# Kernel tuning notes

Hardware: AMD Instinct MI355X
Metric: run time of the kernel (lower is better)

Reference implementation:

```python
import jax, jax.numpy as jnp
import numpy as np

MULTI_INFER_NUM = 8
D_EMBED = 128
N_LAYERS = 2
T, B = 2048, 32


def setup_inputs() -> dict:
    key = jax.random.key(0)
    k1, k2, k3, k4 = jax.random.split(key, 4)
    positions = jax.random.randint(k1, (T, B), 0, 16, dtype=jnp.int64)
    outputs = jax.random.normal(k2, (T, B, D_EMBED), dtype=jnp.float32)
    # 4 LinearTransferFeatures per layer (self_forget, logit, logit_forget, out_forget)
    Ws = jax.random.normal(k3, (N_LAYERS, 4, MULTI_INFER_NUM + 1, D_EMBED, D_EMBED), dtype=jnp.float32) * 0.05
    bs = jax.random.normal(k4, (N_LAYERS, 4, MULTI_INFER_NUM + 1, D_EMBED), dtype=jnp.float32) * 0.05
    return {"positions": positions, "outputs": outputs, "Ws": Ws, "bs": bs}


def _linear(x, onehot, W, b):
    # x: [t,b,d]; onehot: [t,b,e]; W: [e,d,f]; b: [e,d]
    # Equivalent to gathering W[r_pos] ([t,b,d,f]) then einsum('ibde,ibd->ibe'),
    # but computed as per-expert GEMMs + one-hot combine (grouped-GEMM form).
    y_all = jnp.einsum('tbd,edf->tbef', x, W)      # per-expert outputs
    y = jnp.einsum('tbef,tbe->tbf', y_all, onehot)  # select token's expert
    return y + jnp.einsum('tbe,ed->tbd', onehot, b)


def reference(positions, outputs, Ws, bs):
    m = Ws.shape[2] - 1  # multi_infer_num
    r_pos = jnp.where(positions < m, positions, m)
    onehot = jax.nn.one_hot(r_pos, m + 1, dtype=outputs.dtype)
    x = outputs
    for l in range(Ws.shape[0]):
        self_forget = _linear(x, onehot, Ws[l, 0], bs[l, 0])
        logit = _linear(x, onehot, Ws[l, 1], bs[l, 1])
        logit_forget = _linear(x, onehot, Ws[l, 2], bs[l, 2])
        out_forget = _linear(x, onehot, Ws[l, 3], bs[l, 3])
        new_res = x * jax.nn.sigmoid(self_forget) + jnp.tanh(logit) * jax.nn.sigmoid(logit_forget)
        x = jnp.tanh(new_res) * jax.nn.sigmoid(out_forget)
    return x
```

## Files before the change

kernel.cpp:

```cpp
#include <hip/hip_runtime.h>
#include <hip/hip_fp16.h>
#include <stdint.h>

#define TOKENS 65536
#define D      128
#define NEXP   9
#define MT     32
#define MAXTILES (TOKENS / MT + NEXP)
#define NHB    256

typedef _Float16 f16;
typedef _Float16 f16x8  __attribute__((ext_vector_type(8)));
typedef float    f32x4  __attribute__((ext_vector_type(4)));
typedef uint32_t u32;
typedef uint16_t u16;

#define WI_CNT      64
#define ECAP_SMALL  8192
#define ECAP_BIG    49152
#define PERM_U16S   (8 * ECAP_SMALL + ECAP_BIG)
#define WS_PERM_OFF 2048
#define WS_WF_OFF   (WS_PERM_OFF + PERM_U16S * 2)

#define EBASE(E) ((E) < 8 ? ((E) << 13) : 65536)

#define LOG2E  1.44269504f

__global__ void k_pre(const float* __restrict__ Ws, const int* __restrict__ pos,
                      int* __restrict__ wsI, u16* __restrict__ perm16,
                      f16* __restrict__ Wf) {
  const int tid = threadIdx.x;
  if (blockIdx.x >= 256) {
    const int bx  = blockIdx.x - 256;
    const int mat = bx >> 2;
    const int q   = bx & 3;
    const float* src = Ws + (size_t)mat * (D * D);
    f16* dst = Wf + (size_t)mat * (D * D);
#pragma unroll
    for (int p = 0; p < 2; ++p) {
      int cc = q * 512 + p * 256 + tid;
      int ln = cc & 63;
      int kb = (cc >> 6) & 3;
      int c  = cc >> 8;
      int quad = ln >> 4, n = ln & 15;
      int f  = c * 16 + n;
      int d0 = kb * 32 + quad * 8;
      f16x8 w;
#pragma unroll
      for (int i = 0; i < 8; ++i) w[i] = (f16)src[(d0 + i) * D + f];
      *(f16x8*)(dst + cc * 8) = w;
    }
  } else {
    const int b = blockIdx.x;
    const int lane = tid & 63, w = tid >> 6;
    __shared__ int waveCnt[4][NEXP];
    __shared__ int waveBase[4][NEXP];
    __shared__ int blockBase[NEXP];

    int e = pos[b * 256 + tid]; e = e < 8 ? e : 8;
    int myRank = 0;
#pragma unroll
    for (int ee = 0; ee < NEXP; ++ee) {
      unsigned long long m = __ballot(e == ee);
      if (e == ee) myRank = __popcll(m & ((1ull << lane) - 1ull));
      if (lane == 0) waveCnt[w][ee] = __popcll(m);
    }
    __syncthreads();
    if (tid < NEXP) {
      int s = 0;
#pragma unroll
      for (int w2 = 0; w2 < 4; ++w2) { waveBase[w2][tid] = s; s += waveCnt[w2][tid]; }
      blockBase[tid] = atomicAdd(&wsI[WI_CNT + tid * 32], s);
    }
    __syncthreads();
    perm16[EBASE(e) + blockBase[e] + waveBase[w][e] + myRank] = (u16)(b * 256 + tid);
  }
}

__launch_bounds__(256, 4)
__global__ void k_main(const float* __restrict__ xin, const float* __restrict__ bsPtr,
                       const int* __restrict__ wsI, const u16* __restrict__ perm16,
                       const f16* __restrict__ Wf, float* __restrict__ outPtr) {
  __shared__ __attribute__((aligned(16))) f16 Ash[MT][136];
  __shared__ int s_tok[MT];

  const int tid = threadIdx.x;
  const int bid = blockIdx.x;

  int e = 0, tileOffE = 0, cntE = 0, to = 0;
#pragma unroll
  for (int ee = 0; ee < NEXP; ee++) {
    int c = wsI[WI_CNT + ee * 32];
    if (to <= bid) { e = ee; tileOffE = to; cntE = c; }
    to += (c + MT - 1) >> 5;
  }
  if (bid >= to) return;
  const int tokStart   = (bid - tileOffE) * MT;
  const int rowsValid  = min(MT, cntE - tokStart);
  const int permBase   = EBASE(e) + tokStart;

  const int lane = tid & 63;
  const int n    = lane & 15;
  const int quad = lane >> 4;
  const int cBase = (tid >> 6) * 2;
  const int vlane = lane * 8;
  const f16* We = Wf + (size_t)e * 16384;
  const int f0 = cBase * 16 + n;

  f16x8 aF0[4], aF1[4];
  f16x8 b0[4], b1[4], b2[4];

#define PFB(BUF, LL, CC, JJ)                                                   \
  do {                                                                         \
    if ((LL) < 2) {                                                            \
      const f16* _p = We + ((LL) * 4 + (JJ)) * 147456 + (CC) * 2048 + vlane;   \
      _Pragma("unroll")                                                        \
      for (int _kb = 0; _kb < 4; ++_kb)                                        \
        BUF[_kb] = *(const f16x8*)(_p + _kb * 512);                            \
    }                                                                          \
  } while (0)

#define LOAD_AF()                                                              \
  do {                                                                         \
    _Pragma("unroll")                                                          \
    for (int _kb = 0; _kb < 4; ++_kb) {                                        \
      aF0[_kb] = *(const f16x8*)&Ash[n][_kb * 32 + quad * 8];                  \
      aF1[_kb] = *(const f16x8*)&Ash[16 + n][_kb * 32 + quad * 8];             \
    }                                                                          \
  } while (0)

#define MFMA2(G, BUF, BV)                                                      \
  do {                                                                         \
    f32x4 _x = {(BV), (BV), (BV), (BV)};                                       \
    f32x4 _y = _x;                                                             \
    _Pragma("unroll")                                                          \
    for (int _kb = 0; _kb < 4; ++_kb) {                                        \
      _x = __builtin_amdgcn_mfma_f32_16x16x32_f16(aF0[_kb], BUF[_kb], _x, 0, 0, 0); \
      _y = __builtin_amdgcn_mfma_f32_16x16x32_f16(aF1[_kb], BUF[_kb], _y, 0, 0, 0); \
    }                                                                          \
    acc[G][0] = _x; acc[G][1] = _y;                                            \
  } while (0)

  PFB(b0, 0, cBase, 0);
  PFB(b1, 0, cBase, 1);

  float bias[2][2][4];
#pragma unroll
  for (int l = 0; l < 2; ++l)
#pragma unroll
    for (int ci = 0; ci < 2; ++ci)
#pragma unroll
      for (int j = 0; j < 4; ++j)
        bias[l][ci][j] = bsPtr[((l * 4 + j) * NEXP + e) * D + f0 + ci * 16];

  {
    int m = tid >> 3, h = tid & 7;
    bool valid = (m < rowsValid);
    int tok = 0;
    if (valid) tok = (int)perm16[permBase + m];
    if (h == 0) s_tok[m] = valid ? tok : -1;
    const float4* src = (const float4*)(xin + (size_t)tok * D + h * 16);
    f16* drow = &Ash[m][h * 16];
#pragma unroll
    for (int i = 0; i < 2; i++) {
      float4 a = make_float4(0.f, 0.f, 0.f, 0.f), b2v = a;
      if (valid) { a = src[2 * i]; b2v = src[2 * i + 1]; }
      f16x8 wv;
      wv[0] = (f16)a.x;   wv[1] = (f16)a.y;   wv[2] = (f16)a.z;   wv[3] = (f16)a.w;
      wv[4] = (f16)b2v.x; wv[5] = (f16)b2v.y; wv[6] = (f16)b2v.z; wv[7] = (f16)b2v.w;
      *(f16x8*)&drow[i * 8] = wv;
    }
  }
  __syncthreads();
  LOAD_AF();
  __syncthreads();

#define STAGE(L, CI, NLa, NCa, NLb, NCb, BX, BY, BZ)                           \
  do {                                                                         \
    const int cc = cBase + (CI);                                               \
    const int f = f0 + (CI) * 16;                                              \
    f32x4 acc[4][2];                                                           \
    PFB(BZ, L, cc, 2);       MFMA2(0, BX, bias[L][CI][0]);                     \
    PFB(BX, L, cc, 3);       MFMA2(1, BY, bias[L][CI][1]);                     \
    PFB(BY, NLa, NCa, 0);    MFMA2(2, BZ, bias[L][CI][2]);                     \
    PFB(BZ, NLb, NCb, 1);    MFMA2(3, BX, bias[L][CI][3]);                     \
    \
    float xv[2][4];                                                            \
    _Pragma("unroll")                                                          \
    for (int s = 0; s < 2; s++)                                                \
      _Pragma("unroll")                                                        \
      for (int r = 0; r < 4; r++)                                              \
        xv[s][r] = (float)Ash[s * 16 + quad * 4 + r][f];                       \
    _Pragma("unroll")                                                          \
    for (int s = 0; s < 2; s++) {                                              \
      _Pragma("unroll")                                                        \
      for (int r = 0; r < 4; r++) {                                            \
        int m = s * 16 + quad * 4 + r;              \
        float sf = acc[0][s][r];                    \
        float lg = acc[1][s][r];                                               \
        float lf = acc[2][s][r];                                               \
        float of = acc[3][s][r];                                               \
         \
         \
         \
        float Ea = __builtin_amdgcn_exp2f(-LOG2E * sf);                        \
        float Eb = __builtin_amdgcn_exp2f((2.0f * LOG2E) * lg);                \
        float Ec = __builtin_amdgcn_exp2f(-LOG2E * lf);                        \
        float d1 = 1.0f + Ea, d2 = Eb + 1.0f, d3 = 1.0f + Ec;                  \
        float p23 = d2 * d3;                                                   \
        float nr = (xv[s][r] * p23 + (d2 - 2.0f) * d1) *                       \
                   __builtin_amdgcn_rcpf(d1 * p23);                            \
                        \
        float Ed = __builtin_amdgcn_exp2f((2.0f * LOG2E) * nr);                \
        float Ee = __builtin_amdgcn_exp2f(-LOG2E * of);                        \
        float xn = (Ed - 1.0f) * __builtin_amdgcn_rcpf((Ed + 1.0f) * (1.0f + Ee)); \
        if ((L) == 0) {                                                        \
          Ash[m][f] = (f16)xn;                   \
        } else {                                                               \
          int tok = s_tok[m];                                                  \
          if (tok >= 0) outPtr[(size_t)tok * D + f] = xn;                      \
        }                                                                      \
      }                                                                        \
    }                                                                          \
  } while (0)

  STAGE(0, 0, 0, cBase + 1, 0, cBase + 1, b0, b1, b2);
  STAGE(0, 1, 1, cBase,     1, cBase,     b1, b2, b0);
  __syncthreads();
  LOAD_AF();
  STAGE(1, 0, 1, cBase + 1, 1, cBase + 1, b2, b0, b1);
  STAGE(1, 1, 2, 0,         2, 0,         b0, b1, b2);

#undef STAGE
#undef MFMA2
#undef LOAD_AF
#undef PFB
}

extern "C" void kernel_launch(void* const* d_in, const int* in_sizes, int n_in,
                              void* d_out, int out_size, void* d_ws, size_t ws_size,
                              hipStream_t stream) {
  const int*   pos = (const int*)d_in[0];
  const float* x   = (const float*)d_in[1];
  const float* Ws  = (const float*)d_in[2];
  const float* bs  = (const float*)d_in[3];
  float* out = (float*)d_out;
  int* wsI = (int*)d_ws;
  u16* perm16 = (u16*)((char*)d_ws + WS_PERM_OFF);
  f16* Wf = (f16*)((char*)d_ws + WS_WF_OFF);

  hipMemsetAsync((char*)d_ws + WI_CNT * 4, 0, NEXP * 32 * 4, stream);
  k_pre <<<544, 256, 0, stream>>>(Ws, pos, wsI, perm16, Wf);
  k_main<<<MAXTILES, 256, 0, stream>>>(x, bs, wsI, perm16, Wf, out);
}
```

Measured before the change: 125.5 us.

## Make k_main persistent with double-buffered tiles and next-tile prefetch

```diff
diff --git a/kernel.cpp b/kernel.cpp
--- a/kernel.cpp
+++ b/kernel.cpp
@@ -6,7 +6,7 @@
 #define D      128
 #define NEXP   9
 #define MT     32
-#define MAXTILES (TOKENS / MT + NEXP)
+#define NB     768
 #define NHB    256
 
 typedef _Float16 f16;
@@ -77,55 +77,63 @@
   }
 }
 
-__launch_bounds__(256, 4)
+__device__ __forceinline__ void map_tile(const int* __restrict__ wsI, int t,
+                                         int* e, int* permBase, int* rowsValid,
+                                         int* ntiles) {
+  int e_ = 0, tileOff = 0, cnt = 0, to = 0;
+#pragma unroll
+  for (int ee = 0; ee < NEXP; ++ee) {
+    int c = wsI[WI_CNT + ee * 32];
+    if (to <= t) { e_ = ee; tileOff = to; cnt = c; }
+    to += (c + MT - 1) >> 5;
+  }
+  int ts = (t - tileOff) * MT;
+  *e = e_;
+  *permBase = EBASE(e_) + ts;
+  *rowsValid = min(MT, cnt - ts);
+  *ntiles = to;
+}
+
+__launch_bounds__(256, 3)
 __global__ void k_main(const float* __restrict__ xin, const float* __restrict__ bsPtr,
                        const int* __restrict__ wsI, const u16* __restrict__ perm16,
                        const f16* __restrict__ Wf, float* __restrict__ outPtr) {
-  __shared__ __attribute__((aligned(16))) f16 Ash[MT][136];
-  __shared__ int s_tok[MT];
+  __shared__ __attribute__((aligned(16))) f16 Ash[2][MT][136];
+  __shared__ int s_tok[2][MT];
 
   const int tid = threadIdx.x;
   const int bid = blockIdx.x;
-
-  int e = 0, tileOffE = 0, cntE = 0, to = 0;
-#pragma unroll
-  for (int ee = 0; ee < NEXP; ee++) {
-    int c = wsI[WI_CNT + ee * 32];
-    if (to <= bid) { e = ee; tileOffE = to; cntE = c; }
-    to += (c + MT - 1) >> 5;
-  }
-  if (bid >= to) return;
-  const int tokStart   = (bid - tileOffE) * MT;
-  const int rowsValid  = min(MT, cntE - tokStart);
-  const int permBase   = EBASE(e) + tokStart;
 
   const int lane = tid & 63;
   const int n    = lane & 15;
   const int quad = lane >> 4;
   const int cBase = (tid >> 6) * 2;
   const int vlane = lane * 8;
+  const int f0 = cBase * 16 + n;
+  const int mrow = tid >> 3, hcol = tid & 7;
+
+  int e, permBase, rowsValid, ntiles;
+  map_tile(wsI, bid, &e, &permBase, &rowsValid, &ntiles);
+
   const f16* We = Wf + (size_t)e * 16384;
-  const int f0 = cBase * 16 + n;
 
   f16x8 aF0[4], aF1[4];
-  f16x8 b0[4], b1[4], b2[4];
-
-#define PFB(BUF, LL, CC, JJ)                                                   \
+  f16x8 b0[4], b1[4];
+
+#define PFB(BUF, WP, LL, CC, JJ)                                               \
   do {                                                                         \
-    if ((LL) < 2) {                                                            \
-      const f16* _p = We + ((LL) * 4 + (JJ)) * 147456 + (CC) * 2048 + vlane;   \
-      _Pragma("unroll")                                                        \
-      for (int _kb = 0; _kb < 4; ++_kb)                                        \
-        BUF[_kb] = *(const f16x8*)(_p + _kb * 512);                            \
-    }                                                                          \
+    const f16* _p = (WP) + ((LL) * 4 + (JJ)) * 147456 + (CC) * 2048 + vlane;   \
+    _Pragma("unroll")                                                          \
+    for (int _kb = 0; _kb < 4; ++_kb)                                          \
+      BUF[_kb] = *(const f16x8*)(_p + _kb * 512);                              \
   } while (0)
 
-#define LOAD_AF()                                                              \
+#define LOAD_AF(AP)                                                            \
   do {                                                                         \
     _Pragma("unroll")                                                          \
     for (int _kb = 0; _kb < 4; ++_kb) {                                        \
-      aF0[_kb] = *(const f16x8*)&Ash[n][_kb * 32 + quad * 8];                  \
-      aF1[_kb] = *(const f16x8*)&Ash[16 + n][_kb * 32 + quad * 8];             \
+      aF0[_kb] = *(const f16x8*)&AP[n][_kb * 32 + quad * 8];                   \
+      aF1[_kb] = *(const f16x8*)&AP[16 + n][_kb * 32 + quad * 8];              \
     }                                                                          \
   } while (0)
 
@@ -141,8 +149,8 @@
     acc[G][0] = _x; acc[G][1] = _y;                                            \
   } while (0)
 
-  PFB(b0, 0, cBase, 0);
-  PFB(b1, 0, cBase, 1);
+  PFB(b0, We, 0, cBase, 0);
+  PFB(b1, We, 0, cBase, 1);
 
   float bias[2][2][4];
 #pragma unroll
@@ -154,13 +162,12 @@
         bias[l][ci][j] = bsPtr[((l * 4 + j) * NEXP + e) * D + f0 + ci * 16];
 
   {
-    int m = tid >> 3, h = tid & 7;
-    bool valid = (m < rowsValid);
+    bool valid = (mrow < rowsValid);
     int tok = 0;
-    if (valid) tok = (int)perm16[permBase + m];
-    if (h == 0) s_tok[m] = valid ? tok : -1;
-    const float4* src = (const float4*)(xin + (size_t)tok * D + h * 16);
-    f16* drow = &Ash[m][h * 16];
+    if (valid) tok = (int)perm16[permBase + mrow];
+    if (hcol == 0) s_tok[0][mrow] = valid ? tok : -1;
+    const float4* src = (const float4*)(xin + (size_t)tok * D + hcol * 16);
+    f16* drow = &Ash[0][mrow][hcol * 16];
 #pragma unroll
     for (int i = 0; i < 2; i++) {
       float4 a = make_float4(0.f, 0.f, 0.f, 0.f), b2v = a;
@@ -172,25 +179,22 @@
     }
   }
   __syncthreads();
-  LOAD_AF();
-  __syncthreads();
-
-#define STAGE(L, CI, NLa, NCa, NLb, NCb, BX, BY, BZ)                           \
+
+#define STAGE(L, CI, TNL, TNC, WPN)                                            \
   do {                                                                         \
-    const int cc = cBase + (CI);                                               \
     const int f = f0 + (CI) * 16;                                              \
     f32x4 acc[4][2];                                                           \
-    PFB(BZ, L, cc, 2);       MFMA2(0, BX, bias[L][CI][0]);                     \
-    PFB(BX, L, cc, 3);       MFMA2(1, BY, bias[L][CI][1]);                     \
-    PFB(BY, NLa, NCa, 0);    MFMA2(2, BZ, bias[L][CI][2]);                     \
-    PFB(BZ, NLb, NCb, 1);    MFMA2(3, BX, bias[L][CI][3]);                     \
+    PFB(b1, We,  L,   cBase + (CI), 1); MFMA2(0, b0, bias[L][CI][0]);          \
+    PFB(b0, We,  L,   cBase + (CI), 2); MFMA2(1, b1, bias[L][CI][1]);          \
+    PFB(b1, We,  L,   cBase + (CI), 3); MFMA2(2, b0, bias[L][CI][2]);          \
+    PFB(b0, WPN, TNL, TNC,          0); MFMA2(3, b1, bias[L][CI][3]);          \
     \
     float xv[2][4];                                                            \
     _Pragma("unroll")                                                          \
     for (int s = 0; s < 2; s++)                                                \
       _Pragma("unroll")                                                        \
       for (int r = 0; r < 4; r++)                                              \
-        xv[s][r] = (float)Ash[s * 16 + quad * 4 + r][f];                       \
+        xv[s][r] = (float)A[s * 16 + quad * 4 + r][f];                         \
     _Pragma("unroll")                                                          \
     for (int s = 0; s < 2; s++) {                                              \
       _Pragma("unroll")                                                        \
@@ -201,8 +205,6 @@
         float lf = acc[2][s][r];                                               \
         float of = acc[3][s][r];                                               \
          \
-         \
-         \
         float Ea = __builtin_amdgcn_exp2f(-LOG2E * sf);                        \
         float Eb = __builtin_amdgcn_exp2f((2.0f * LOG2E) * lg);                \
         float Ec = __builtin_amdgcn_exp2f(-LOG2E * lf);                        \
@@ -210,27 +212,86 @@
         float p23 = d2 * d3;                                                   \
         float nr = (xv[s][r] * p23 + (d2 - 2.0f) * d1) *                       \
                    __builtin_amdgcn_rcpf(d1 * p23);                            \
-                        \
         float Ed = __builtin_amdgcn_exp2f((2.0f * LOG2E) * nr);                \
         float Ee = __builtin_amdgcn_exp2f(-LOG2E * of);                        \
         float xn = (Ed - 1.0f) * __builtin_amdgcn_rcpf((Ed + 1.0f) * (1.0f + Ee)); \
         if ((L) == 0) {                                                        \
-          Ash[m][f] = (f16)xn;                   \
+          A[m][f] = (f16)xn;                     \
         } else {                                                               \
-          int tok = s_tok[m];                                                  \
+          int tok = s_tokC[m];                                                 \
           if (tok >= 0) outPtr[(size_t)tok * D + f] = xn;                      \
         }                                                                      \
       }                                                                        \
     }                                                                          \
   } while (0)
 
-  STAGE(0, 0, 0, cBase + 1, 0, cBase + 1, b0, b1, b2);
-  STAGE(0, 1, 1, cBase,     1, cBase,     b1, b2, b0);
-  __syncthreads();
-  LOAD_AF();
-  STAGE(1, 0, 1, cBase + 1, 1, cBase + 1, b2, b0, b1);
-  STAGE(1, 1, 2, 0,         2, 0,         b0, b1, b2);
-
+  int cur = 0;
+#pragma unroll 1
+  for (int t = bid; ; t += NB) {
+    f16 (*A)[136] = Ash[cur];
+    int* s_tokC = s_tok[cur];
+
+    LOAD_AF(A);
+    __syncthreads();
+
+    const bool hasNext = (t + NB) < ntiles;
+    const f16* WeN = We;
+    int e2 = e, tok2 = 0; bool v2 = false;
+    float4 xa, xb, xc, xd;
+    float bias2[2][2][4];
+    if (hasNext) {
+      int pb2, rv2, nt2;
+      map_tile(wsI, t + NB, &e2, &pb2, &rv2, &nt2);
+      WeN = Wf + (size_t)e2 * 16384;
+      v2 = (mrow < rv2);
+      tok2 = v2 ? (int)perm16[pb2 + mrow] : 0;
+      const float4* src = (const float4*)(xin + (size_t)tok2 * D + hcol * 16);
+      xa = src[0]; xb = src[1]; xc = src[2]; xd = src[3];
+#pragma unroll
+      for (int l = 0; l < 2; ++l)
+#pragma unroll
+        for (int ci = 0; ci < 2; ++ci)
+#pragma unroll
+          for (int j = 0; j < 4; ++j)
+            bias2[l][ci][j] = bsPtr[((l * 4 + j) * NEXP + e2) * D + f0 + ci * 16];
+    }
+
+    STAGE(0, 0, 0, cBase + 1, We);
+    STAGE(0, 1, 1, cBase,     We);
+    __syncthreads();
+    LOAD_AF(A);
+    STAGE(1, 0, 1, cBase + 1, We);
+
+    if (hasNext) {
+      if (!v2) {
+        xa = make_float4(0.f, 0.f, 0.f, 0.f);
+        xb = xa; xc = xa; xd = xa;
+      }
+      if (hcol == 0) s_tok[cur ^ 1][mrow] = v2 ? tok2 : -1;
+      f16x8 w0, w1;
+      w0[0] = (f16)xa.x; w0[1] = (f16)xa.y; w0[2] = (f16)xa.z; w0[3] = (f16)xa.w;
+      w0[4] = (f16)xb.x; w0[5] = (f16)xb.y; w0[6] = (f16)xb.z; w0[7] = (f16)xb.w;
+      w1[0] = (f16)xc.x; w1[1] = (f16)xc.y; w1[2] = (f16)xc.z; w1[3] = (f16)xc.w;
+      w1[4] = (f16)xd.x; w1[5] = (f16)xd.y; w1[6] = (f16)xd.z; w1[7] = (f16)xd.w;
+      f16* drow = &Ash[cur ^ 1][mrow][hcol * 16];
+      *(f16x8*)&drow[0] = w0;
+      *(f16x8*)&drow[8] = w1;
+    }
+
+    STAGE(1, 1, 0, cBase, WeN);
+
+    if (!hasNext) return;
+    __syncthreads();
+
+#pragma unroll
+    for (int l = 0; l < 2; ++l)
+#pragma unroll
+      for (int ci = 0; ci < 2; ++ci)
+#pragma unroll
+        for (int j = 0; j < 4; ++j)
+          bias[l][ci][j] = bias2[l][ci][j];
+    We = WeN; e = e2; cur ^= 1;
+  }
 #undef STAGE
 #undef MFMA2
 #undef LOAD_AF
@@ -251,5 +312,5 @@
 
   hipMemsetAsync((char*)d_ws + WI_CNT * 4, 0, NEXP * 32 * 4, stream);
   k_pre <<<544, 256, 0, stream>>>(Ws, pos, wsI, perm16, Wf);
-  k_main<<<MAXTILES, 256, 0, stream>>>(x, bs, wsI, perm16, Wf, out);
+  k_main<<<NB, 256, 0, stream>>>(x, bs, wsI, perm16, Wf, out);
 }
```

New measurement: 128.3 us. 2.2% more time.

## Stage final outputs in shared memory and write coalesced float4 rows; use double-buffered weights

Applied to the files above, without the earlier changes.

```diff
diff --git a/kernel.cpp b/kernel.cpp
--- a/kernel.cpp
+++ b/kernel.cpp
@@ -82,6 +82,7 @@
                        const int* __restrict__ wsI, const u16* __restrict__ perm16,
                        const f16* __restrict__ Wf, float* __restrict__ outPtr) {
   __shared__ __attribute__((aligned(16))) f16 Ash[MT][136];
+  __shared__ __attribute__((aligned(16))) float Osh[MT][132];
   __shared__ int s_tok[MT];
 
   const int tid = threadIdx.x;
@@ -108,7 +109,7 @@
   const int f0 = cBase * 16 + n;
 
   f16x8 aF0[4], aF1[4];
-  f16x8 b0[4], b1[4], b2[4];
+  f16x8 b0[4], b1[4];
 
 #define PFB(BUF, LL, CC, JJ)                                                   \
   do {                                                                         \
@@ -175,15 +176,15 @@
   LOAD_AF();
   __syncthreads();
 
-#define STAGE(L, CI, NLa, NCa, NLb, NCb, BX, BY, BZ)                           \
+#define STAGE(L, CI, NL, NC)                                                   \
   do {                                                                         \
     const int cc = cBase + (CI);                                               \
     const int f = f0 + (CI) * 16;                                              \
     f32x4 acc[4][2];                                                           \
-    PFB(BZ, L, cc, 2);       MFMA2(0, BX, bias[L][CI][0]);                     \
-    PFB(BX, L, cc, 3);       MFMA2(1, BY, bias[L][CI][1]);                     \
-    PFB(BY, NLa, NCa, 0);    MFMA2(2, BZ, bias[L][CI][2]);                     \
-    PFB(BZ, NLb, NCb, 1);    MFMA2(3, BX, bias[L][CI][3]);                     \
+    PFB(b1, L, cc, 1);  MFMA2(0, b0, bias[L][CI][0]);                          \
+    PFB(b0, L, cc, 2);  MFMA2(1, b1, bias[L][CI][1]);                          \
+    PFB(b1, L, cc, 3);  MFMA2(2, b0, bias[L][CI][2]);                          \
+    PFB(b0, NL, NC, 0); MFMA2(3, b1, bias[L][CI][3]);                          \
     \
     float xv[2][4];                                                            \
     _Pragma("unroll")                                                          \
@@ -201,8 +202,6 @@
         float lf = acc[2][s][r];                                               \
         float of = acc[3][s][r];                                               \
          \
-         \
-         \
         float Ea = __builtin_amdgcn_exp2f(-LOG2E * sf);                        \
         float Eb = __builtin_amdgcn_exp2f((2.0f * LOG2E) * lg);                \
         float Ec = __builtin_amdgcn_exp2f(-LOG2E * lf);                        \
@@ -210,27 +209,40 @@
         float p23 = d2 * d3;                                                   \
         float nr = (xv[s][r] * p23 + (d2 - 2.0f) * d1) *                       \
                    __builtin_amdgcn_rcpf(d1 * p23);                            \
-                        \
         float Ed = __builtin_amdgcn_exp2f((2.0f * LOG2E) * nr);                \
         float Ee = __builtin_amdgcn_exp2f(-LOG2E * of);                        \
         float xn = (Ed - 1.0f) * __builtin_amdgcn_rcpf((Ed + 1.0f) * (1.0f + Ee)); \
         if ((L) == 0) {                                                        \
           Ash[m][f] = (f16)xn;                   \
         } else {                                                               \
-          int tok = s_tok[m];                                                  \
-          if (tok >= 0) outPtr[(size_t)tok * D + f] = xn;                      \
+          Osh[m][f] = xn;                         \
         }                                                                      \
       }                                                                        \
     }                                                                          \
   } while (0)
 
-  STAGE(0, 0, 0, cBase + 1, 0, cBase + 1, b0, b1, b2);
-  STAGE(0, 1, 1, cBase,     1, cBase,     b1, b2, b0);
+  STAGE(0, 0, 0, cBase + 1);
+  STAGE(0, 1, 1, cBase);
   __syncthreads();
   LOAD_AF();
-  STAGE(1, 0, 1, cBase + 1, 1, cBase + 1, b2, b0, b1);
-  STAGE(1, 1, 2, 0,         2, 0,         b0, b1, b2);
-
+  STAGE(1, 0, 1, cBase + 1);
+  STAGE(1, 1, 2, 0);
+
+  __syncthreads();
+
+  {
+    const int c4 = tid & 31;
+    const int r0 = tid >> 5;
+#pragma unroll
+    for (int k = 0; k < 4; ++k) {
+      int m = r0 + k * 8;
+      int tok = s_tok[m];
+      if (tok >= 0) {
+        float4 v = *(const float4*)&Osh[m][c4 * 4];
+        *(float4*)(outPtr + (size_t)tok * D + c4 * 4) = v;
+      }
+    }
+  }
 #undef STAGE
 #undef MFMA2
 #undef LOAD_AF
```

Measured after the change: 129.7 us. 1.03x slower.
